# Kernel tuning notes

Measured on AMD Instinct MI355X. Metric: run time of the kernel, lower is better.

## Reference

```python
import jax, jax.numpy as jnp
import numpy as np
from math import sqrt

N = 50000      # n_nodes
M = 800000     # n_edges (avg degree 16)
D = 256        # d_Embedding
H = 8          # heads
DK = 32        # per-head key/query dim
DV = 32        # per-head value dim


def setup_inputs() -> dict:
    key = jax.random.key(0)
    ks = jax.random.split(key, 10)
    s = 0.02
    x = jax.random.normal(ks[0], (N, D), dtype=jnp.float32)
    edge_index = jax.random.randint(ks[1], (2, M), 0, N, dtype=jnp.int32)
    # projection weights stored pre-reshaped to (D, H, dhead); equivalent to nn.Linear(D, H*dhead)
    Wk = jax.random.normal(ks[2], (D, H, DK), dtype=jnp.float32) * s
    bk = jax.random.normal(ks[3], (H, DK), dtype=jnp.float32) * s
    Wq = jax.random.normal(ks[4], (D, H, DK), dtype=jnp.float32) * s
    bq = jax.random.normal(ks[5], (H, DK), dtype=jnp.float32) * s
    Wv = jax.random.normal(ks[6], (D, H, DV), dtype=jnp.float32) * s
    bv = jax.random.normal(ks[7], (H, DV), dtype=jnp.float32) * s
    Wagg = jax.random.normal(ks[8], (H * DV, D), dtype=jnp.float32) * s
    bagg = jnp.zeros((D,), dtype=jnp.float32)
    Wff = jax.random.normal(ks[9], (D, D), dtype=jnp.float32) * s
    bff = jnp.zeros((D,), dtype=jnp.float32)
    return {"x": x, "edge_index": edge_index, "Wk": Wk, "bk": bk, "Wq": Wq,
            "bq": bq, "Wv": Wv, "bv": bv, "Wagg": Wagg, "bagg": bagg,
            "Wff": Wff, "bff": bff}


def reference(x, edge_index, Wk, bk, Wq, bq, Wv, bv, Wagg, bagg, Wff, bff):
    recv = edge_index[0]
    send = edge_index[1]
    # per-head projections: (N, H, d)
    K = jnp.einsum('nd,dhk->nhk', x, Wk) + bk
    Q = jnp.einsum('nd,dhk->nhk', x, Wq) + bq
    V = jnp.einsum('nd,dhv->nhv', x, Wv) + bv
    # edge-wise attention logits: (M, H)
    qk = jnp.sum(Q[recv] * K[send], axis=-1)
    # faithful to original: rescale by 3/global_max, then exp
    att = jnp.exp(qk * 3.0 / jnp.max(qk))
    # segment-softmax normalization over edges sharing a receiver
    sums = jax.ops.segment_sum(att, recv, num_segments=N)  # (N, H)
    att = att / sums[recv] / sqrt(DK)
    # weighted scatter-add of sender values: (N, H, DV)
    msg = att[..., None] * V[send]
    out = jax.ops.segment_sum(msg, recv, num_segments=N)
    out = jax.nn.relu(out).reshape(N, H * DV)
    out = jax.nn.relu(out @ Wagg + bagg)
    out = jax.nn.relu(out @ Wff + bff)
    return x + out
```

## Files before the change

### kernel.cpp

```cpp
#include <hip/hip_runtime.h>

#define N_NODES 50000
#define M_EDGES 800000

typedef __bf16 bf16x8 __attribute__((ext_vector_type(8)));
typedef __bf16 bf16x4 __attribute__((ext_vector_type(4)));
typedef float  f32x4  __attribute__((ext_vector_type(4)));

static __device__ __forceinline__ unsigned enc_ord(float f) {
    unsigned b = __float_as_uint(f);
    return (b & 0x80000000u) ? ~b : (b | 0x80000000u);
}
static __device__ __forceinline__ float dec_ord(unsigned u) {
    unsigned b = (u & 0x80000000u) ? (u ^ 0x80000000u) : ~u;
    return __uint_as_float(b);
}
static __device__ __forceinline__ float bf2f(unsigned short u) {
    return __uint_as_float(((unsigned)u) << 16);
}

__global__ void init_kernel(int* counts, int* cursor, unsigned* gmax) {
    int t = blockIdx.x * blockDim.x + threadIdx.x;
    if (t < N_NODES) { counts[t] = 0; cursor[t] = 0; }
    if (t == 0) *gmax = 0u;
}

__global__ void wsplit_kernel(const float* __restrict__ W,
                              __bf16* __restrict__ th, __bf16* __restrict__ tl) {
    int t = blockIdx.x * 256 + threadIdx.x;
    int n = t >> 8, k = t & 255;
    float v = W[(size_t)k * 256 + n];
    __bf16 h = (__bf16)v;
    th[t] = h;
    tl[t] = (__bf16)(v - (float)h);
}

__global__ __launch_bounds__(256) void gemm_mfma(
    const float* __restrict__ A,
    const __bf16* __restrict__ Bth, const __bf16* __restrict__ Btl,
    const float* __restrict__ bias, const float* __restrict__ residual,
    float* __restrict__ C, __bf16* __restrict__ Cb, int nrows, int do_relu) {
    __shared__ __attribute__((aligned(16))) __bf16 sAh[128 * 40];
    __shared__ __attribute__((aligned(16))) __bf16 sAl[128 * 40];
    __shared__ __attribute__((aligned(16))) __bf16 sBh[128 * 40];
    __shared__ __attribute__((aligned(16))) __bf16 sBl[128 * 40];

    int row0 = blockIdx.x * 128;
    int n0   = blockIdx.y * 128;
    int tid  = threadIdx.x;
    int lane = tid & 63, wave = tid >> 6;
    int wm = (wave >> 1) * 64, wn = (wave & 1) * 64;

    f32x4 acc[4][4];
    #pragma unroll
    for (int i = 0; i < 4; i++)
        #pragma unroll
        for (int j = 0; j < 4; j++) acc[i][j] = (f32x4)(0.f);

    int r  = tid >> 1;
    int hf = tid & 1;

    for (int kk = 0; kk < 256; kk += 32) {
        {
            const float* ap = A + (size_t)(row0 + r) * 256 + kk + hf * 16;
            bool valid = (row0 + r) < nrows;
            #pragma unroll
            for (int q = 0; q < 4; q++) {
                float4 v = valid ? *(const float4*)(ap + q * 4)
                                 : make_float4(0.f, 0.f, 0.f, 0.f);
                bf16x4 hh, ll;
                hh[0] = (__bf16)v.x; ll[0] = (__bf16)(v.x - (float)hh[0]);
                hh[1] = (__bf16)v.y; ll[1] = (__bf16)(v.y - (float)hh[1]);
                hh[2] = (__bf16)v.z; ll[2] = (__bf16)(v.z - (float)hh[2]);
                hh[3] = (__bf16)v.w; ll[3] = (__bf16)(v.w - (float)hh[3]);
                *(bf16x4*)&sAh[r * 40 + hf * 16 + q * 4] = hh;
                *(bf16x4*)&sAl[r * 40 + hf * 16 + q * 4] = ll;
            }
        }
        {
            size_t gb = (size_t)(n0 + r) * 256 + kk + hf * 16;
            uint4 vh0 = *(const uint4*)(Bth + gb);
            uint4 vh1 = *(const uint4*)(Bth + gb + 8);
            uint4 vl0 = *(const uint4*)(Btl + gb);
            uint4 vl1 = *(const uint4*)(Btl + gb + 8);
            *(uint4*)&sBh[r * 40 + hf * 16]     = vh0;
            *(uint4*)&sBh[r * 40 + hf * 16 + 8] = vh1;
            *(uint4*)&sBl[r * 40 + hf * 16]     = vl0;
            *(uint4*)&sBl[r * 40 + hf * 16 + 8] = vl1;
        }
        __syncthreads();

        int m_base = wm + (lane & 15);
        int n_base = wn + (lane & 15);
        int koff = (lane >> 4) * 8;
        bf16x8 ah[4], al[4], bh[4], bl[4];
        #pragma unroll
        for (int mt = 0; mt < 4; mt++) {
            ah[mt] = *(const bf16x8*)&sAh[(m_base + mt * 16) * 40 + koff];
            al[mt] = *(const bf16x8*)&sAl[(m_base + mt * 16) * 40 + koff];
        }
        #pragma unroll
        for (int nt = 0; nt < 4; nt++) {
            bh[nt] = *(const bf16x8*)&sBh[(n_base + nt * 16) * 40 + koff];
            bl[nt] = *(const bf16x8*)&sBl[(n_base + nt * 16) * 40 + koff];
        }
        #pragma unroll
        for (int mt = 0; mt < 4; mt++)
            #pragma unroll
            for (int nt = 0; nt < 4; nt++) {
                acc[mt][nt] = __builtin_amdgcn_mfma_f32_16x16x32_bf16(ah[mt], bh[nt], acc[mt][nt], 0, 0, 0);
                acc[mt][nt] = __builtin_amdgcn_mfma_f32_16x16x32_bf16(al[mt], bh[nt], acc[mt][nt], 0, 0, 0);
                acc[mt][nt] = __builtin_amdgcn_mfma_f32_16x16x32_bf16(ah[mt], bl[nt], acc[mt][nt], 0, 0, 0);
            }
        __syncthreads();
    }

    #pragma unroll
    for (int mt = 0; mt < 4; mt++) {
        #pragma unroll
        for (int nt = 0; nt < 4; nt++) {
            int col = n0 + wn + nt * 16 + (lane & 15);
            #pragma unroll
            for (int rr = 0; rr < 4; rr++) {
                int row = row0 + wm + mt * 16 + (lane >> 4) * 4 + rr;
                if (row < nrows) {
                    float v = acc[mt][nt][rr] + bias[col];
                    if (do_relu) v = fmaxf(v, 0.f);
                    if (Cb) {
                        Cb[(size_t)row * 256 + col] = (__bf16)v;
                    } else {
                        if (residual) v += residual[(size_t)row * 256 + col];
                        C[(size_t)row * 256 + col] = v;
                    }
                }
            }
        }
    }
}

__global__ void hist_kernel(const int* __restrict__ recv, int* __restrict__ counts) {
    int t = blockIdx.x * 256 + threadIdx.x;
    if (t < M_EDGES) atomicAdd(&counts[recv[t]], 1);
}

__global__ void scan_kernel(const int* __restrict__ counts, int* __restrict__ offsets) {
    __shared__ int part[256];
    int t = threadIdx.x;
    const int per = (N_NODES + 255) / 256;
    int start = t * per;
    int end = min(start + per, N_NODES);
    int s = 0;
    for (int i = start; i < end; i++) s += counts[i];
    part[t] = s;
    __syncthreads();
    if (t == 0) {
        int acc = 0;
        for (int i = 0; i < 256; i++) { int v = part[i]; part[i] = acc; acc += v; }
    }
    __syncthreads();
    int acc = part[t];
    for (int i = start; i < end; i++) { offsets[i] = acc; acc += counts[i]; }
    if (end == N_NODES && start < N_NODES) offsets[N_NODES] = acc;
}

__global__ void fill_kernel(const int* __restrict__ recv, const int* __restrict__ send,
                            const int* __restrict__ offsets,
                            int* __restrict__ cursor, int* __restrict__ ssorted) {
    int t = blockIdx.x * 256 + threadIdx.x;
    if (t < M_EDGES) {
        int r = recv[t];
        int pos = offsets[r] + atomicAdd(&cursor[r], 1);
        ssorted[pos] = send[t];
    }
}

__global__ __launch_bounds__(256) void qk_csr_kernel(
    const int* __restrict__ offsets, const int* __restrict__ ssorted,
    const float* __restrict__ Q, const unsigned short* __restrict__ Kb,
    float* __restrict__ qks, unsigned* __restrict__ gmax) {
    __shared__ float swmax[4];
    int wave = threadIdx.x >> 6, lane = threadIdx.x & 63;
    int n = blockIdx.x * 4 + wave;
    float wmax = -INFINITY;
    if (n < N_NODES) {
        int off = offsets[n], deg = offsets[n + 1] - off;
        float4 q = *(const float4*)(Q + (size_t)n * 256 + lane * 4);
        if (deg > 0) {
            int s0 = ssorted[off];
            ushort4 kv = *(const ushort4*)(Kb + (size_t)s0 * 256 + lane * 4);
            for (int j = 0; j < deg; j++) {
                ushort4 kc = kv;
                if (j + 1 < deg) {
                    int s1 = ssorted[off + j + 1];
                    kv = *(const ushort4*)(Kb + (size_t)s1 * 256 + lane * 4);
                }
                float d = q.x * bf2f(kc.x) + q.y * bf2f(kc.y)
                        + q.z * bf2f(kc.z) + q.w * bf2f(kc.w);
                d += __shfl_xor(d, 1);
                d += __shfl_xor(d, 2);
                d += __shfl_xor(d, 4);
                if ((lane & 7) == 0) qks[(size_t)(off + j) * 8 + (lane >> 3)] = d;
                wmax = fmaxf(wmax, d);
            }
        }
    }
    wmax = fmaxf(wmax, __shfl_xor(wmax, 8));
    wmax = fmaxf(wmax, __shfl_xor(wmax, 16));
    wmax = fmaxf(wmax, __shfl_xor(wmax, 32));
    if (lane == 0) swmax[wave] = wmax;
    __syncthreads();
    if (threadIdx.x == 0) {
        float m = fmaxf(fmaxf(swmax[0], swmax[1]), fmaxf(swmax[2], swmax[3]));
        if (m > -INFINITY) atomicMax(gmax, enc_ord(m));
    }
}

__global__ __launch_bounds__(256) void node_agg_kernel(
    const int* __restrict__ offsets, const int* __restrict__ ssorted,
    const float* __restrict__ qks, const unsigned short* __restrict__ Vb,
    const unsigned* __restrict__ gmax, float* __restrict__ msg) {
    __shared__ int   s_send[32];
    __shared__ float s_att[32][8];
    int n = blockIdx.x;
    int c = threadIdx.x;
    int h = c >> 5;
    int off = offsets[n];
    int deg = offsets[n + 1] - off;
    float scale = 3.0f / dec_ord(*gmax);
    float sum = 0.f, acc = 0.f;
    for (int i0 = 0; i0 < deg; i0 += 32) {
        int cn = min(32, deg - i0);
        __syncthreads();
        if (c < cn) s_send[c] = ssorted[off + i0 + c];
        if (c < cn * 8) {
            s_att[c >> 3][c & 7] = __expf(qks[(size_t)(off + i0) * 8 + c] * scale);
        }
        __syncthreads();
        #pragma unroll 4
        for (int i = 0; i < cn; i++) {
            float a = s_att[i][h];
            sum += a;
            acc += a * bf2f(Vb[(size_t)s_send[i] * 256 + c]);
        }
    }
    float inv = (deg > 0) ? 1.0f / (sum * 5.65685424949238f) : 0.f;
    msg[(size_t)n * 256 + c] = fmaxf(acc * inv, 0.f);
}

extern "C" void kernel_launch(void* const* d_in, const int* in_sizes, int n_in,
                              void* d_out, int out_size, void* d_ws, size_t ws_size,
                              hipStream_t stream) {
    const float* x    = (const float*)d_in[0];
    const int*   edge = (const int*)d_in[1];
    const int*   recv = edge;
    const int*   send = edge + M_EDGES;
    const float* Wk   = (const float*)d_in[2];
    const float* bk   = (const float*)d_in[3];
    const float* Wq   = (const float*)d_in[4];
    const float* bq   = (const float*)d_in[5];
    const float* Wv   = (const float*)d_in[6];
    const float* bv   = (const float*)d_in[7];
    const float* Wagg = (const float*)d_in[8];
    const float* bagg = (const float*)d_in[9];
    const float* Wff  = (const float*)d_in[10];
    const float* bff  = (const float*)d_in[11];
    float* out = (float*)d_out;

    float*  Qbuf  = (float*)d_ws;
    float*  msg   = Qbuf + (size_t)N_NODES * 256;
    float*  qks   = msg + (size_t)N_NODES * 256;
    __bf16* Kbf   = (__bf16*)(qks + (size_t)M_EDGES * 8);
    __bf16* Vbf   = Kbf + (size_t)N_NODES * 256;
    int* counts   = (int*)(Vbf + (size_t)N_NODES * 256);
    int* cursor   = counts + N_NODES;
    int* offsets  = cursor + N_NODES;
    int* ssorted  = offsets + N_NODES + 1;
    unsigned* gmax = (unsigned*)(ssorted + M_EDGES);
    __bf16* wt    = (__bf16*)(gmax + 1);
    __bf16* WkH = wt;              __bf16* WkL = wt + 65536;
    __bf16* WqH = wt + 2 * 65536;  __bf16* WqL = wt + 3 * 65536;
    __bf16* WvH = wt + 4 * 65536;  __bf16* WvL = wt + 5 * 65536;
    __bf16* WaH = wt + 6 * 65536;  __bf16* WaL = wt + 7 * 65536;
    __bf16* WfH = wt + 8 * 65536;  __bf16* WfL = wt + 9 * 65536;
    float* hidden = Qbuf;

    dim3 blk(256);
    dim3 gemm_grid((N_NODES + 127) / 128, 2);
    dim3 edge_grid((M_EDGES + 255) / 256);

    hipLaunchKernelGGL(init_kernel, dim3((N_NODES + 255) / 256), blk, 0, stream,
                       counts, cursor, gmax);
    hipLaunchKernelGGL(wsplit_kernel, dim3(256), blk, 0, stream, Wk,   WkH, WkL);
    hipLaunchKernelGGL(wsplit_kernel, dim3(256), blk, 0, stream, Wq,   WqH, WqL);
    hipLaunchKernelGGL(wsplit_kernel, dim3(256), blk, 0, stream, Wv,   WvH, WvL);
    hipLaunchKernelGGL(wsplit_kernel, dim3(256), blk, 0, stream, Wagg, WaH, WaL);
    hipLaunchKernelGGL(wsplit_kernel, dim3(256), blk, 0, stream, Wff,  WfH, WfL);
    hipLaunchKernelGGL(gemm_mfma, gemm_grid, blk, 0, stream, x, WkH, WkL, bk, nullptr,
                       (float*)nullptr, Kbf, N_NODES, 0);
    hipLaunchKernelGGL(gemm_mfma, gemm_grid, blk, 0, stream, x, WqH, WqL, bq, nullptr,
                       Qbuf, (__bf16*)nullptr, N_NODES, 0);
    hipLaunchKernelGGL(gemm_mfma, gemm_grid, blk, 0, stream, x, WvH, WvL, bv, nullptr,
                       (float*)nullptr, Vbf, N_NODES, 0);
    hipLaunchKernelGGL(hist_kernel, edge_grid, blk, 0, stream, recv, counts);
    hipLaunchKernelGGL(scan_kernel, dim3(1), blk, 0, stream, counts, offsets);
    hipLaunchKernelGGL(fill_kernel, edge_grid, blk, 0, stream, recv, send, offsets, cursor, ssorted);
    hipLaunchKernelGGL(qk_csr_kernel, dim3((N_NODES + 3) / 4), blk, 0, stream,
                       offsets, ssorted, Qbuf, (const unsigned short*)Kbf, qks, gmax);
    hipLaunchKernelGGL(node_agg_kernel, dim3(N_NODES), blk, 0, stream,
                       offsets, ssorted, qks, (const unsigned short*)Vbf, gmax, msg);
    hipLaunchKernelGGL(gemm_mfma, gemm_grid, blk, 0, stream, msg, WaH, WaL, bagg, nullptr,
                       hidden, (__bf16*)nullptr, N_NODES, 1);
    hipLaunchKernelGGL(gemm_mfma, gemm_grid, blk, 0, stream, hidden, WfH, WfL, bff, x,
                       out, (__bf16*)nullptr, N_NODES, 1);
}
```

Measured before the change: 902.1 us.

## Process two edges per wave in qk and split node aggregation across waves

The qk kernel now has each half-wave handle a separate edge, loading 8 bf16 K values per lane with 16-byte loads and prefetching K rows two steps ahead. The node aggregation kernel drops the shared-memory staging loop. Each of its 4 waves takes every fourth edge, computes exp inline, accumulates 4 channels per lane from 8-byte V loads, and the partial sums are combined through shared memory at the end. The aim is more memory-level parallelism and fewer barriers on the gather-bound edge loops. The cost is extra shared-memory reduction and redundant exp work per lane.

```diff
diff --git a/kernel.cpp b/kernel.cpp
--- a/kernel.cpp
+++ b/kernel.cpp
@@ -15,9 +15,8 @@
     unsigned b = (u & 0x80000000u) ? (u ^ 0x80000000u) : ~u;
     return __uint_as_float(b);
 }
-static __device__ __forceinline__ float bf2f(unsigned short u) {
-    return __uint_as_float(((unsigned)u) << 16);
-}
+static __device__ __forceinline__ float bflo(unsigned u) { return __uint_as_float(u << 16); }
+static __device__ __forceinline__ float bfhi(unsigned u) { return __uint_as_float(u & 0xffff0000u); }
 
 __global__ void init_kernel(int* counts, int* cursor, unsigned* gmax) {
     int t = blockIdx.x * blockDim.x + threadIdx.x;
@@ -180,30 +179,39 @@
     float* __restrict__ qks, unsigned* __restrict__ gmax) {
     __shared__ float swmax[4];
     int wave = threadIdx.x >> 6, lane = threadIdx.x & 63;
+    int e_slot = lane >> 5;
+    int sl = lane & 31;
     int n = blockIdx.x * 4 + wave;
     float wmax = -INFINITY;
     if (n < N_NODES) {
         int off = offsets[n], deg = offsets[n + 1] - off;
-        float4 q = *(const float4*)(Q + (size_t)n * 256 + lane * 4);
+        float4 qa = *(const float4*)(Q + (size_t)n * 256 + sl * 8);
+        float4 qb = *(const float4*)(Q + (size_t)n * 256 + sl * 8 + 4);
         if (deg > 0) {
-            int s0 = ssorted[off];
-            ushort4 kv = *(const ushort4*)(Kb + (size_t)s0 * 256 + lane * 4);
-            for (int j = 0; j < deg; j++) {
-                ushort4 kc = kv;
-                if (j + 1 < deg) {
-                    int s1 = ssorted[off + j + 1];
-                    kv = *(const ushort4*)(Kb + (size_t)s1 * 256 + lane * 4);
-                }
-                float d = q.x * bf2f(kc.x) + q.y * bf2f(kc.y)
-                        + q.z * bf2f(kc.z) + q.w * bf2f(kc.w);
+            int npairs = (deg + 1) >> 1;
+            int s_cur = (e_slot < deg) ? ssorted[off + e_slot] : 0;
+            int s_nxt = (2 + e_slot < deg) ? ssorted[off + 2 + e_slot] : 0;
+            uint4 kv_cur = *(const uint4*)(Kb + (size_t)s_cur * 256 + sl * 8);
+            for (int p = 0; p < npairs; p++) {
+                int jf = p * 2 + 4 + e_slot;
+                int s2 = (jf < deg) ? ssorted[off + jf] : 0;
+                uint4 kv_nxt = *(const uint4*)(Kb + (size_t)s_nxt * 256 + sl * 8);
+                int jc = p * 2 + e_slot;
+                float d = qa.x * bflo(kv_cur.x) + qa.y * bfhi(kv_cur.x)
+                        + qa.z * bflo(kv_cur.y) + qa.w * bfhi(kv_cur.y)
+                        + qb.x * bflo(kv_cur.z) + qb.y * bfhi(kv_cur.z)
+                        + qb.z * bflo(kv_cur.w) + qb.w * bfhi(kv_cur.w);
                 d += __shfl_xor(d, 1);
                 d += __shfl_xor(d, 2);
-                d += __shfl_xor(d, 4);
-                if ((lane & 7) == 0) qks[(size_t)(off + j) * 8 + (lane >> 3)] = d;
-                wmax = fmaxf(wmax, d);
+                if (jc < deg) {
+                    wmax = fmaxf(wmax, d);
+                    if ((sl & 3) == 0) qks[(size_t)(off + jc) * 8 + (sl >> 2)] = d;
+                }
+                kv_cur = kv_nxt; s_nxt = s2;
             }
         }
     }
+    wmax = fmaxf(wmax, __shfl_xor(wmax, 4));
     wmax = fmaxf(wmax, __shfl_xor(wmax, 8));
     wmax = fmaxf(wmax, __shfl_xor(wmax, 16));
     wmax = fmaxf(wmax, __shfl_xor(wmax, 32));
@@ -219,31 +227,42 @@
     const int* __restrict__ offsets, const int* __restrict__ ssorted,
     const float* __restrict__ qks, const unsigned short* __restrict__ Vb,
     const unsigned* __restrict__ gmax, float* __restrict__ msg) {
-    __shared__ int   s_send[32];
-    __shared__ float s_att[32][8];
+    __shared__ float s_part[4][256];
+    __shared__ float s_sums[4][8];
     int n = blockIdx.x;
-    int c = threadIdx.x;
-    int h = c >> 5;
+    int j = threadIdx.x >> 6;
+    int l = threadIdx.x & 63;
+    int h = l >> 3;
     int off = offsets[n];
     int deg = offsets[n + 1] - off;
     float scale = 3.0f / dec_ord(*gmax);
-    float sum = 0.f, acc = 0.f;
-    for (int i0 = 0; i0 < deg; i0 += 32) {
-        int cn = min(32, deg - i0);
-        __syncthreads();
-        if (c < cn) s_send[c] = ssorted[off + i0 + c];
-        if (c < cn * 8) {
-            s_att[c >> 3][c & 7] = __expf(qks[(size_t)(off + i0) * 8 + c] * scale);
-        }
-        __syncthreads();
-        #pragma unroll 4
-        for (int i = 0; i < cn; i++) {
-            float a = s_att[i][h];
+    float sum = 0.f;
+    float a0 = 0.f, a1 = 0.f, a2 = 0.f, a3 = 0.f;
+    if (j < deg) {
+        int s_cur = ssorted[off + j];
+        int s_nxt = (j + 4 < deg) ? ssorted[off + j + 4] : 0;
+        float qv_cur = qks[(size_t)(off + j) * 8 + h];
+        uint2 v_cur = *(const uint2*)(Vb + (size_t)s_cur * 256 + l * 4);
+        for (int i = j; i < deg; i += 4) {
+            int i2 = i + 8;
+            int s2 = (i2 < deg) ? ssorted[off + i2] : 0;
+            float qv_nxt = (i + 4 < deg) ? qks[(size_t)(off + i + 4) * 8 + h] : 0.f;
+            uint2 v_nxt = *(const uint2*)(Vb + (size_t)s_nxt * 256 + l * 4);
+            float a = __expf(qv_cur * scale);
             sum += a;
-            acc += a * bf2f(Vb[(size_t)s_send[i] * 256 + c]);
-        }
-    }
-    float inv = (deg > 0) ? 1.0f / (sum * 5.65685424949238f) : 0.f;
+            a0 += a * bflo(v_cur.x); a1 += a * bfhi(v_cur.x);
+            a2 += a * bflo(v_cur.y); a3 += a * bfhi(v_cur.y);
+            v_cur = v_nxt; s_nxt = s2; qv_cur = qv_nxt;
+        }
+    }
+    *(float4*)&s_part[j][l * 4] = make_float4(a0, a1, a2, a3);
+    if ((l & 7) == 0) s_sums[j][h] = sum;
+    __syncthreads();
+    int c = threadIdx.x;
+    int ch = c >> 5;
+    float tot = s_sums[0][ch] + s_sums[1][ch] + s_sums[2][ch] + s_sums[3][ch];
+    float acc = s_part[0][c] + s_part[1][c] + s_part[2][c] + s_part[3][c];
+    float inv = (deg > 0) ? 1.0f / (tot * 5.65685424949238f) : 0.f;
     msg[(size_t)n * 256 + c] = fmaxf(acc * inv, 0.f);
 }
 
```

Result: no change. 885.4 us (-1.9%).

## Edge-parallel QK scores and wave-per-node persistent aggregation with prefetch

Applied to the files above, without the earlier changes.

The QK kernel moves from one wave per receiver node to an edge-parallel layout. A new receiver-sorted index array, stored in the msg buffer, is filled alongside the sender array, and each wave processes two edges per step across a persistent grid, which balances load against degree variance. The aggregation kernel moves from one 256-thread block per node to one wave per node with 4 channels per lane. It uses shuffle-broadcast sender indices, software-prefetches V rows and scores two edges ahead, and drops shared memory and barriers. The cost is an extra int write per edge, redundant Q row loads per edge in place of one per node, and fewer threads in flight per node.

```diff
diff --git a/kernel.cpp b/kernel.cpp
--- a/kernel.cpp
+++ b/kernel.cpp
@@ -15,9 +15,8 @@
     unsigned b = (u & 0x80000000u) ? (u ^ 0x80000000u) : ~u;
     return __uint_as_float(b);
 }
-static __device__ __forceinline__ float bf2f(unsigned short u) {
-    return __uint_as_float(((unsigned)u) << 16);
-}
+static __device__ __forceinline__ float bflo(unsigned u) { return __uint_as_float(u << 16); }
+static __device__ __forceinline__ float bfhi(unsigned u) { return __uint_as_float(u & 0xffff0000u); }
 
 __global__ void init_kernel(int* counts, int* cursor, unsigned* gmax) {
     int t = blockIdx.x * blockDim.x + threadIdx.x;
@@ -165,86 +164,105 @@
 
 __global__ void fill_kernel(const int* __restrict__ recv, const int* __restrict__ send,
                             const int* __restrict__ offsets,
-                            int* __restrict__ cursor, int* __restrict__ ssorted) {
+                            int* __restrict__ cursor, int* __restrict__ ssorted,
+                            int* __restrict__ rsorted) {
     int t = blockIdx.x * 256 + threadIdx.x;
     if (t < M_EDGES) {
         int r = recv[t];
         int pos = offsets[r] + atomicAdd(&cursor[r], 1);
         ssorted[pos] = send[t];
+        rsorted[pos] = r;
     }
 }
 
 __global__ __launch_bounds__(256) void qk_csr_kernel(
-    const int* __restrict__ offsets, const int* __restrict__ ssorted,
+    const int* __restrict__ ssorted, const int* __restrict__ rsorted,
     const float* __restrict__ Q, const unsigned short* __restrict__ Kb,
     float* __restrict__ qks, unsigned* __restrict__ gmax) {
-    __shared__ float swmax[4];
-    int wave = threadIdx.x >> 6, lane = threadIdx.x & 63;
-    int n = blockIdx.x * 4 + wave;
+    int wave_id = (blockIdx.x * 256 + threadIdx.x) >> 6;
+    int lane = threadIdx.x & 63;
+    int e_slot = lane >> 5;
+    int sl = lane & 31;
+    const int nwaves = (gridDim.x * 256) >> 6;
+    const int npairs = M_EDGES / 2;
     float wmax = -INFINITY;
-    if (n < N_NODES) {
-        int off = offsets[n], deg = offsets[n + 1] - off;
-        float4 q = *(const float4*)(Q + (size_t)n * 256 + lane * 4);
-        if (deg > 0) {
-            int s0 = ssorted[off];
-            ushort4 kv = *(const ushort4*)(Kb + (size_t)s0 * 256 + lane * 4);
-            for (int j = 0; j < deg; j++) {
-                ushort4 kc = kv;
-                if (j + 1 < deg) {
-                    int s1 = ssorted[off + j + 1];
-                    kv = *(const ushort4*)(Kb + (size_t)s1 * 256 + lane * 4);
-                }
-                float d = q.x * bf2f(kc.x) + q.y * bf2f(kc.y)
-                        + q.z * bf2f(kc.z) + q.w * bf2f(kc.w);
-                d += __shfl_xor(d, 1);
-                d += __shfl_xor(d, 2);
-                d += __shfl_xor(d, 4);
-                if ((lane & 7) == 0) qks[(size_t)(off + j) * 8 + (lane >> 3)] = d;
-                wmax = fmaxf(wmax, d);
-            }
-        }
-    }
+    for (int pp = wave_id; pp < npairs; pp += 2 * nwaves) {
+        int ppB = pp + nwaves;
+        bool hasB = ppB < npairs;
+        int pA = pp * 2 + e_slot;
+        int pB = (hasB ? ppB * 2 : pp * 2) + e_slot;
+        int sA = ssorted[pA], rA = rsorted[pA];
+        int sB = ssorted[pB], rB = rsorted[pB];
+        uint4 kA = *(const uint4*)(Kb + (size_t)sA * 256 + sl * 8);
+        uint4 kB = *(const uint4*)(Kb + (size_t)sB * 256 + sl * 8);
+        float4 qaA = *(const float4*)(Q + (size_t)rA * 256 + sl * 8);
+        float4 qbA = *(const float4*)(Q + (size_t)rA * 256 + sl * 8 + 4);
+        float4 qaB = *(const float4*)(Q + (size_t)rB * 256 + sl * 8);
+        float4 qbB = *(const float4*)(Q + (size_t)rB * 256 + sl * 8 + 4);
+        float dA = qaA.x * bflo(kA.x) + qaA.y * bfhi(kA.x)
+                 + qaA.z * bflo(kA.y) + qaA.w * bfhi(kA.y)
+                 + qbA.x * bflo(kA.z) + qbA.y * bfhi(kA.z)
+                 + qbA.z * bflo(kA.w) + qbA.w * bfhi(kA.w);
+        float dB = qaB.x * bflo(kB.x) + qaB.y * bfhi(kB.x)
+                 + qaB.z * bflo(kB.y) + qaB.w * bfhi(kB.y)
+                 + qbB.x * bflo(kB.z) + qbB.y * bfhi(kB.z)
+                 + qbB.z * bflo(kB.w) + qbB.w * bfhi(kB.w);
+        dA += __shfl_xor(dA, 1); dA += __shfl_xor(dA, 2);
+        dB += __shfl_xor(dB, 1); dB += __shfl_xor(dB, 2);
+        wmax = fmaxf(wmax, fmaxf(dA, dB));
+        if ((sl & 3) == 0) {
+            qks[(size_t)pA * 8 + (sl >> 2)] = dA;
+            if (hasB) qks[(size_t)pB * 8 + (sl >> 2)] = dB;
+        }
+    }
+    wmax = fmaxf(wmax, __shfl_xor(wmax, 1));
+    wmax = fmaxf(wmax, __shfl_xor(wmax, 2));
+    wmax = fmaxf(wmax, __shfl_xor(wmax, 4));
     wmax = fmaxf(wmax, __shfl_xor(wmax, 8));
     wmax = fmaxf(wmax, __shfl_xor(wmax, 16));
     wmax = fmaxf(wmax, __shfl_xor(wmax, 32));
-    if (lane == 0) swmax[wave] = wmax;
-    __syncthreads();
-    if (threadIdx.x == 0) {
-        float m = fmaxf(fmaxf(swmax[0], swmax[1]), fmaxf(swmax[2], swmax[3]));
-        if (m > -INFINITY) atomicMax(gmax, enc_ord(m));
-    }
+    if (lane == 0 && wmax > -INFINITY) atomicMax(gmax, enc_ord(wmax));
 }
 
 __global__ __launch_bounds__(256) void node_agg_kernel(
     const int* __restrict__ offsets, const int* __restrict__ ssorted,
     const float* __restrict__ qks, const unsigned short* __restrict__ Vb,
     const unsigned* __restrict__ gmax, float* __restrict__ msg) {
-    __shared__ int   s_send[32];
-    __shared__ float s_att[32][8];
-    int n = blockIdx.x;
-    int c = threadIdx.x;
-    int h = c >> 5;
-    int off = offsets[n];
-    int deg = offsets[n + 1] - off;
+    int wave_id = (blockIdx.x * 256 + threadIdx.x) >> 6;
+    int lane = threadIdx.x & 63;
+    int h = lane >> 3;
+    const int nwaves = (gridDim.x * 256) >> 6;
     float scale = 3.0f / dec_ord(*gmax);
-    float sum = 0.f, acc = 0.f;
-    for (int i0 = 0; i0 < deg; i0 += 32) {
-        int cn = min(32, deg - i0);
-        __syncthreads();
-        if (c < cn) s_send[c] = ssorted[off + i0 + c];
-        if (c < cn * 8) {
-            s_att[c >> 3][c & 7] = __expf(qks[(size_t)(off + i0) * 8 + c] * scale);
-        }
-        __syncthreads();
-        #pragma unroll 4
-        for (int i = 0; i < cn; i++) {
-            float a = s_att[i][h];
-            sum += a;
-            acc += a * bf2f(Vb[(size_t)s_send[i] * 256 + c]);
-        }
-    }
-    float inv = (deg > 0) ? 1.0f / (sum * 5.65685424949238f) : 0.f;
-    msg[(size_t)n * 256 + c] = fmaxf(acc * inv, 0.f);
+    for (int n = wave_id; n < N_NODES; n += nwaves) {
+        int off = offsets[n];
+        int deg = offsets[n + 1] - off;
+        float sum = 0.f, a0 = 0.f, a1 = 0.f, a2 = 0.f, a3 = 0.f;
+        for (int b = 0; b < deg; b += 64) {
+            int bn = min(64, deg - b);
+            int idxb = ssorted[off + b + min(lane, bn - 1)];
+            #define VROW(i) (*(const uint2*)(Vb + \
+                (size_t)__shfl(idxb, min((i), bn - 1)) * 256 + lane * 4))
+            #define QKL(i) qks[(size_t)(off + b + min((i), bn - 1)) * 8 + h]
+            uint2 v0 = VROW(0);
+            uint2 v1 = VROW(1);
+            float q0 = QKL(0);
+            float q1 = QKL(1);
+            for (int i = 0; i < bn; i++) {
+                uint2 vc = v0; v0 = v1; v1 = VROW(i + 2);
+                float qc = q0; q0 = q1; q1 = QKL(i + 2);
+                float a = __expf(qc * scale);
+                sum += a;
+                a0 += a * bflo(vc.x); a1 += a * bfhi(vc.x);
+                a2 += a * bflo(vc.y); a3 += a * bfhi(vc.y);
+            }
+            #undef VROW
+            #undef QKL
+        }
+        float inv = (deg > 0) ? 1.0f / (sum * 5.65685424949238f) : 0.f;
+        *(float4*)(msg + (size_t)n * 256 + lane * 4) =
+            make_float4(fmaxf(a0 * inv, 0.f), fmaxf(a1 * inv, 0.f),
+                        fmaxf(a2 * inv, 0.f), fmaxf(a3 * inv, 0.f));
+    }
 }
 
 extern "C" void kernel_launch(void* const* d_in, const int* in_sizes, int n_in,
@@ -282,6 +300,7 @@
     __bf16* WvH = wt + 4 * 65536;  __bf16* WvL = wt + 5 * 65536;
     __bf16* WaH = wt + 6 * 65536;  __bf16* WaL = wt + 7 * 65536;
     __bf16* WfH = wt + 8 * 65536;  __bf16* WfL = wt + 9 * 65536;
+    int* rsorted  = (int*)msg;
     float* hidden = Qbuf;
 
     dim3 blk(256);
@@ -303,10 +322,11 @@
                        (float*)nullptr, Vbf, N_NODES, 0);
     hipLaunchKernelGGL(hist_kernel, edge_grid, blk, 0, stream, recv, counts);
     hipLaunchKernelGGL(scan_kernel, dim3(1), blk, 0, stream, counts, offsets);
-    hipLaunchKernelGGL(fill_kernel, edge_grid, blk, 0, stream, recv, send, offsets, cursor, ssorted);
-    hipLaunchKernelGGL(qk_csr_kernel, dim3((N_NODES + 3) / 4), blk, 0, stream,
-                       offsets, ssorted, Qbuf, (const unsigned short*)Kbf, qks, gmax);
-    hipLaunchKernelGGL(node_agg_kernel, dim3(N_NODES), blk, 0, stream,
+    hipLaunchKernelGGL(fill_kernel, edge_grid, blk, 0, stream, recv, send, offsets,
+                       cursor, ssorted, rsorted);
+    hipLaunchKernelGGL(qk_csr_kernel, dim3(1024), blk, 0, stream,
+                       ssorted, rsorted, Qbuf, (const unsigned short*)Kbf, qks, gmax);
+    hipLaunchKernelGGL(node_agg_kernel, dim3(1024), blk, 0, stream,
                        offsets, ssorted, qks, (const unsigned short*)Vbf, gmax, msg);
     hipLaunchKernelGGL(gemm_mfma, gemm_grid, blk, 0, stream, msg, WaH, WaL, bagg, nullptr,
                        hidden, (__bf16*)nullptr, N_NODES, 1);
```

New measurement: 870.0 us. -3.6%, faster.
